# Kernel tuning notes

Hardware: AMD Instinct MI355X
Metric: run time of the kernel (lower is better)

Reference implementation:

```python
import jax, jax.numpy as jnp
import numpy as np

B, T, C, H = 1, 4096, 768, 12
D = C // H  # head_dim = 64


def setup_inputs() -> dict:
    key = jax.random.key(0)
    ks = jax.random.split(key, 5)
    s = 1.0 / np.sqrt(C)
    return {
        "x": jax.random.normal(ks[0], (B, T, C), dtype=jnp.float32),
        "Wq": jax.random.normal(ks[1], (C, C), dtype=jnp.float32) * s,
        "bq": jnp.zeros((C,), dtype=jnp.float32),
        "Wk": jax.random.normal(ks[2], (C, C), dtype=jnp.float32) * s,
        "bk": jnp.zeros((C,), dtype=jnp.float32),
        "Wv": jax.random.normal(ks[3], (C, C), dtype=jnp.float32) * s,
        "bv": jnp.zeros((C,), dtype=jnp.float32),
        "Wo": jax.random.normal(ks[4], (C, C), dtype=jnp.float32) * s,
        "bo": jnp.zeros((C,), dtype=jnp.float32),
    }


def reference(x, Wq, bq, Wk, bk, Wv, bv, Wo, bo):
    # Linear projections (torch nn.Linear: y = x @ W.T + b)
    q = (x @ Wq.T + bq).reshape(B, T, H, D).transpose(0, 2, 1, 3)  # [B,H,T,D]
    k = (x @ Wk.T + bk).reshape(B, T, H, D).transpose(0, 2, 1, 3)
    v = (x @ Wv.T + bv).reshape(B, T, H, D).transpose(0, 2, 1, 3)
    scale = 1.0 / jnp.sqrt(jnp.asarray(D, dtype=x.dtype))
    scores = jnp.einsum("bhqd,bhkd->bhqk", q, k) * scale  # [B,H,T,T]
    attn = jax.nn.softmax(scores, axis=-1)
    out = jnp.einsum("bhqk,bhkd->bhqd", attn, v)  # [B,H,T,D]
    y = out.transpose(0, 2, 1, 3).reshape(B, T, C)
    return y @ Wo.T + bo
```

## Files before the change

### kernel.cpp

```cpp
#include <hip/hip_runtime.h>
#include <math.h>

#define T_ 4096
#define C_ 768
#define H_ 12
#define D_ 64
#define TC_ ((size_t)T_ * C_)
#define CC_ ((size_t)C_ * C_)

typedef __attribute__((ext_vector_type(8))) __bf16 bf16x8;
typedef __attribute__((ext_vector_type(4))) __bf16 bf16x4;
typedef __attribute__((ext_vector_type(2))) __bf16 bf16x2;
typedef __attribute__((ext_vector_type(4))) float f32x4;
typedef __attribute__((ext_vector_type(16))) float f32x16;
typedef __attribute__((ext_vector_type(8))) unsigned short u16x8;
typedef __attribute__((ext_vector_type(4))) unsigned int u32x4;


static __device__ __forceinline__ float fast_exp2(float x) {
#if __has_builtin(__builtin_amdgcn_exp2f)
    return __builtin_amdgcn_exp2f(x);
#else
    return exp2f(x);
#endif
}

static __device__ __forceinline__ unsigned pack2(float a, float b) {
    bf16x2 v = { (__bf16)a, (__bf16)b };
    return __builtin_bit_cast(unsigned, v);
}

static __device__ __forceinline__ void gload16(const void* g, void* l) {
    __builtin_amdgcn_global_load_lds(
        (const __attribute__((address_space(1))) unsigned int*)g,
        (__attribute__((address_space(3))) unsigned int*)l, 16, 0, 0);
}

__global__ void f2b_kernel(const float* __restrict__ in,
                           unsigned short* __restrict__ out, int n4) {
    int i = blockIdx.x * blockDim.x + threadIdx.x;
    const int stride = gridDim.x * blockDim.x;
    for (; i < n4; i += stride) {
        float4 v = ((const float4*)in)[i];
        bf16x4 o = { (__bf16)v.x, (__bf16)v.y, (__bf16)v.z, (__bf16)v.w };
        *(bf16x4*)&out[(size_t)i * 4] = o;
    }
}

__global__ void f2b4_kernel(const float* __restrict__ w0, const float* __restrict__ w1,
                            const float* __restrict__ w2, const float* __restrict__ w3,
                            unsigned short* __restrict__ out) {
    const float* src = (blockIdx.y == 0) ? w0 : (blockIdx.y == 1) ? w1
                     : (blockIdx.y == 2) ? w2 : w3;
    unsigned short* dst = out + (size_t)blockIdx.y * CC_;
    const int i = blockIdx.x * blockDim.x + threadIdx.x;
    float4 v = ((const float4*)src)[i];
    bf16x4 o = { (__bf16)v.x, (__bf16)v.y, (__bf16)v.z, (__bf16)v.w };
    *(bf16x4*)&dst[(size_t)i * 4] = o;
}

#define BM 128
#define BN 128
#define BKG 64

struct GemmRegs {
    const unsigned short* ag[4];
    const unsigned short* wg[4];
    unsigned short* la[4];
    unsigned short* lw[4];
    int lq, lg, wr, wc;
};

static __device__ __forceinline__ void gemm_setup(
    GemmRegs& R, const unsigned short* A, const unsigned short* W,
    unsigned short* Asm, unsigned short* Bsm, int bm, int bn, int K)
{
    const int tid = threadIdx.x;
    const int wave = tid >> 6, lane = tid & 63;
    R.lq = lane & 15; R.lg = lane >> 4;
    R.wr = wave >> 1; R.wc = wave & 1;
#pragma unroll
    for (int i = 0; i < 4; ++i) {
        const int flat = wave * 256 + i * 64 + lane;
        const int row = flat >> 3;
        const int col = ((flat & 7) * 8) ^ ((row & 7) << 3);
        R.ag[i] = A + (size_t)(bm + row) * K + col;
        R.wg[i] = W + (size_t)(bn + row) * K + col;
        R.la[i] = Asm + (wave * 4 + i) * 512;
        R.lw[i] = Bsm + (wave * 4 + i) * 512;
    }
}

static __device__ __forceinline__ void gemm_loop(
    GemmRegs& R, unsigned short* Asm, unsigned short* Bsm, int K, f32x4 acc[4][4])
{
    const int sw = (R.lq & 7) << 3;
    int colA[2];
#pragma unroll
    for (int ks = 0; ks < 2; ++ks)
        colA[ks] = (ks * 32 + R.lg * 8) ^ sw;
    for (int kb = 0; kb < K; kb += BKG) {
        __syncthreads();
#pragma unroll
        for (int i = 0; i < 4; ++i) {
            gload16(R.ag[i] + kb, R.la[i]);
            gload16(R.wg[i] + kb, R.lw[i]);
        }
        __syncthreads();
        __builtin_amdgcn_s_setprio(1);
#pragma unroll
        for (int ks = 0; ks < 2; ++ks) {
            bf16x8 af[4], wf[4];
#pragma unroll
            for (int m = 0; m < 4; ++m)
                af[m] = *(const bf16x8*)&Asm[(R.wr * 64 + m * 16 + R.lq) * BKG + colA[ks]];
#pragma unroll
            for (int n = 0; n < 4; ++n)
                wf[n] = *(const bf16x8*)&Bsm[(R.wc * 64 + n * 16 + R.lq) * BKG + colA[ks]];
#pragma unroll
            for (int m = 0; m < 4; ++m)
#pragma unroll
                for (int n = 0; n < 4; ++n)
                    acc[m][n] = __builtin_amdgcn_mfma_f32_16x16x32_bf16(af[m], wf[n], acc[m][n], 0, 0, 0);
        }
        __builtin_amdgcn_s_setprio(0);
    }
}

__global__ __launch_bounds__(256) void qkv128(
    const unsigned short* __restrict__ xb,
    const unsigned short* __restrict__ Wqb, const unsigned short* __restrict__ Wkb,
    const unsigned short* __restrict__ Wvb,
    const float* __restrict__ bq, const float* __restrict__ bk, const float* __restrict__ bv,
    unsigned short* __restrict__ Qb, unsigned short* __restrict__ Kb,
    unsigned short* __restrict__ Vtb)
{
    __shared__ unsigned short Asm[BM * BKG];
    __shared__ unsigned short Bsm[BN * BKG];
    const int z = blockIdx.z;
    const unsigned short* W = (z == 0) ? Wqb : (z == 1) ? Wkb : Wvb;
    const float* bias = (z == 0) ? bq : (z == 1) ? bk : bv;
    const int bm = blockIdx.x * BM, bn = blockIdx.y * BN;

    GemmRegs R;
    gemm_setup(R, xb, W, Asm, Bsm, bm, bn, C_);
    f32x4 acc[4][4] = {};
    gemm_loop(R, Asm, Bsm, C_, acc);

    const float sc = (z == 0) ? 0.18033688011112042f : 1.0f;
#pragma unroll
    for (int mt = 0; mt < 4; ++mt) {
        const int m0 = bm + R.wr * 64 + mt * 16 + R.lg * 4;
#pragma unroll
        for (int nt = 0; nt < 4; ++nt) {
            const int n = bn + R.wc * 64 + nt * 16 + R.lq;
            const float b = bias[n];
            if (z == 2) {
                const int tp = (m0 & ~12) | ((m0 & 4) << 1) | ((m0 & 8) >> 1);
                bf16x4 o = { (__bf16)(acc[mt][nt][0] + b), (__bf16)(acc[mt][nt][1] + b),
                             (__bf16)(acc[mt][nt][2] + b), (__bf16)(acc[mt][nt][3] + b) };
                *(bf16x4*)&Vtb[(size_t)n * T_ + tp] = o;
            } else {
                unsigned short* Y = (z == 0) ? Qb : Kb;
#pragma unroll
                for (int r = 0; r < 4; ++r)
                    Y[(size_t)(m0 + r) * C_ + n] =
                        __builtin_bit_cast(unsigned short, (__bf16)((acc[mt][nt][r] + b) * sc));
            }
        }
    }
}

__global__ __launch_bounds__(256) void out128(
    const unsigned short* __restrict__ ctxb, const unsigned short* __restrict__ Wob,
    const float* __restrict__ bo, float* __restrict__ out)
{
    __shared__ unsigned short Asm[BM * BKG];
    __shared__ unsigned short Bsm[BN * BKG];
    const int bm = blockIdx.x * BM, bn = blockIdx.y * BN;

    GemmRegs R;
    gemm_setup(R, ctxb, Wob, Asm, Bsm, bm, bn, C_);
    f32x4 acc[4][4] = {};
    gemm_loop(R, Asm, Bsm, C_, acc);

#pragma unroll
    for (int mt = 0; mt < 4; ++mt) {
        const int m0 = bm + R.wr * 64 + mt * 16 + R.lg * 4;
#pragma unroll
        for (int nt = 0; nt < 4; ++nt) {
            const int n = bn + R.wc * 64 + nt * 16 + R.lq;
            const float b = bo[n];
#pragma unroll
            for (int r = 0; r < 4; ++r)
                out[(size_t)(m0 + r) * C_ + n] = acc[mt][nt][r] + b;
        }
    }
}

#define SPLITS 2
#define KVTILES (T_ / 64 / SPLITS)

__global__ __launch_bounds__(256, 3) void attn32s(
    const unsigned short* __restrict__ Qb, const unsigned short* __restrict__ Kb,
    const unsigned short* __restrict__ Vtb, unsigned short* __restrict__ Opart,
    float* __restrict__ lpart)
{
    __shared__ unsigned short Ks[2][64 * 64];
    __shared__ unsigned short Vs[2][64 * 64];

    const int tid = threadIdx.x;
    const int wave = tid >> 6, lane = tid & 63;
    const int lq = lane & 31, hi = lane >> 5;

    const int bid = blockIdx.x;
    const int sw = (bid & 7) * 96 + (bid >> 3);
    const int split = sw / 384;
    const int rem = sw - split * 384;
    const int h = rem >> 5, qt = rem & 31;
    const int q0 = qt * 128 + wave * 32;
    const int kv0 = split * (T_ / SPLITS);

    const int swz = (lq & 7) << 4;
    int rof[4];
#pragma unroll
    for (int ks = 0; ks < 4; ++ks)
        rof[ks] = lq * 128 + ((hi * 16 + ks * 32) ^ swz);

    bf16x8 qf[4];
    {
        const unsigned short* qp = Qb + (size_t)(q0 + lq) * C_ + h * D_ + hi * 8;
#pragma unroll
        for (int ks = 0; ks < 4; ++ks) qf[ks] = *(const bf16x8*)(qp + ks * 16);
    }

    const char* gk[2];
    const char* gv[2];
    char* kds[2];
    char* vds[2];
#pragma unroll
    for (int j = 0; j < 2; ++j) {
        const int f = j * 256 + tid;
        const int row = f >> 3;
        const int col = (f & 7) * 16;
        gk[j] = (const char*)Kb + (size_t)(kv0 + row) * (C_ * 2) + h * (D_ * 2) + col;
        gv[j] = (const char*)Vtb + (size_t)(h * D_ + row) * (T_ * 2) + kv0 * 2 + col;
        kds[j] = (char*)&Ks[0][0] + row * 128 + (col ^ ((row & 7) << 4));
        vds[j] = (char*)&Vs[0][0] + row * 128 + (col ^ ((row & 7) << 4));
    }

    u16x8 kreg[2], vreg[2];
#pragma unroll
    for (int j = 0; j < 2; ++j) {
        kreg[j] = *(const u16x8*)(gk[j]);
        vreg[j] = *(const u16x8*)(gv[j]);
    }
#pragma unroll
    for (int j = 0; j < 2; ++j) {
        *(u16x8*)kds[j] = kreg[j];
        *(u16x8*)vds[j] = vreg[j];
    }
    __syncthreads();
#pragma unroll
    for (int j = 0; j < 2; ++j) {
        kreg[j] = *(const u16x8*)(gk[j] + 64 * (C_ * 2));
        vreg[j] = *(const u16x8*)(gv[j] + 128);
    }

    f32x16 oacc0 = {}, oacc1 = {};
    float lrun = 0.f;

    for (int it = 0; it < KVTILES; ++it) {
        const int cur = it & 1;
        const char* kb = (const char*)&Ks[cur][0];
        const char* vb = (const char*)&Vs[cur][0];

        f32x16 s0 = {}, s1 = {};
        __builtin_amdgcn_s_setprio(1);
#pragma unroll
        for (int ks = 0; ks < 4; ++ks) {
            bf16x8 kf0 = *(const bf16x8*)(kb + rof[ks]);
            bf16x8 kf1 = *(const bf16x8*)(kb + 4096 + rof[ks]);
            s0 = __builtin_amdgcn_mfma_f32_32x32x16_bf16(kf0, qf[ks], s0, 0, 0, 0);
            s1 = __builtin_amdgcn_mfma_f32_32x32x16_bf16(kf1, qf[ks], s1, 0, 0, 0);
        }
        __builtin_amdgcn_s_setprio(0);

#pragma unroll
        for (int r = 0; r < 16; ++r) {
            s0[r] = fast_exp2(s0[r]);
            s1[r] = fast_exp2(s1[r]);
        }
        {
            float ps[8];
#pragma unroll
            for (int r = 0; r < 8; ++r)
                ps[r] = (s0[r] + s0[r + 8]) + (s1[r] + s1[r + 8]);
            ps[0] += ps[4]; ps[1] += ps[5]; ps[2] += ps[6]; ps[3] += ps[7];
            float pt = (ps[0] + ps[1]) + (ps[2] + ps[3]);
            lrun += pt + __shfl_xor(pt, 32);
        }

        bf16x8 pf[4];
        {
            u32x4 a0 = { pack2(s0[0], s0[1]), pack2(s0[2], s0[3]),
                         pack2(s0[4], s0[5]), pack2(s0[6], s0[7]) };
            pf[0] = __builtin_bit_cast(bf16x8, a0);
            u32x4 a1 = { pack2(s0[8], s0[9]), pack2(s0[10], s0[11]),
                         pack2(s0[12], s0[13]), pack2(s0[14], s0[15]) };
            pf[1] = __builtin_bit_cast(bf16x8, a1);
            u32x4 a2 = { pack2(s1[0], s1[1]), pack2(s1[2], s1[3]),
                         pack2(s1[4], s1[5]), pack2(s1[6], s1[7]) };
            pf[2] = __builtin_bit_cast(bf16x8, a2);
            u32x4 a3 = { pack2(s1[8], s1[9]), pack2(s1[10], s1[11]),
                         pack2(s1[12], s1[13]), pack2(s1[14], s1[15]) };
            pf[3] = __builtin_bit_cast(bf16x8, a3);
        }

        __builtin_amdgcn_s_setprio(1);
#pragma unroll
        for (int ks = 0; ks < 4; ++ks) {
            bf16x8 vf0 = *(const bf16x8*)(vb + rof[ks]);
            bf16x8 vf1 = *(const bf16x8*)(vb + 4096 + rof[ks]);
            oacc0 = __builtin_amdgcn_mfma_f32_32x32x16_bf16(vf0, pf[ks], oacc0, 0, 0, 0);
            oacc1 = __builtin_amdgcn_mfma_f32_32x32x16_bf16(vf1, pf[ks], oacc1, 0, 0, 0);
        }
        __builtin_amdgcn_s_setprio(0);

        if (it + 1 < KVTILES) {
            const int nxt = (cur ^ 1) * 8192;
#pragma unroll
            for (int j = 0; j < 2; ++j) {
                *(u16x8*)(kds[j] + nxt) = kreg[j];
                *(u16x8*)(vds[j] + nxt) = vreg[j];
            }
            if (it + 2 < KVTILES) {
                const size_t ko = (size_t)(it + 2) * 64 * (C_ * 2);
                const size_t vo = (size_t)(it + 2) * 128;
#pragma unroll
                for (int j = 0; j < 2; ++j) {
                    kreg[j] = *(const u16x8*)(gk[j] + ko);
                    vreg[j] = *(const u16x8*)(gv[j] + vo);
                }
            }
        }
        __syncthreads();
    }

    unsigned short* op = Opart + ((size_t)(split * H_ + h) * T_ + q0 + lq) * 64;
#pragma unroll
    for (int k = 0; k < 4; ++k) {
        bf16x4 o0 = { (__bf16)oacc0[4 * k + 0], (__bf16)oacc0[4 * k + 1],
                      (__bf16)oacc0[4 * k + 2], (__bf16)oacc0[4 * k + 3] };
        *(bf16x4*)&op[8 * k + 4 * hi] = o0;
        bf16x4 o1 = { (__bf16)oacc1[4 * k + 0], (__bf16)oacc1[4 * k + 1],
                      (__bf16)oacc1[4 * k + 2], (__bf16)oacc1[4 * k + 3] };
        *(bf16x4*)&op[32 + 8 * k + 4 * hi] = o1;
    }
    if (hi == 0)
        lpart[(size_t)(split * H_ + h) * T_ + q0 + lq] = lrun;
}

__global__ __launch_bounds__(256) void combine2(
    const unsigned short* __restrict__ Opart, const float* __restrict__ lpart,
    unsigned short* __restrict__ ctxb)
{
    const int idx = blockIdx.x * 256 + threadIdx.x;
    const int dq = idx & 15;
    const int ht = idx >> 4;
    const int h = ht >> 12;
    const int t = ht & (T_ - 1);

    const float l0 = lpart[(size_t)h * T_ + t];
    const float l1 = lpart[(size_t)(H_ + h) * T_ + t];
    const float inv = 1.f / (l0 + l1);
    const bf16x4 a0 = *(const bf16x4*)&Opart[((size_t)h * T_ + t) * 64 + dq * 4];
    const bf16x4 a1 = *(const bf16x4*)&Opart[((size_t)(H_ + h) * T_ + t) * 64 + dq * 4];
    bf16x4 r;
#pragma unroll
    for (int i = 0; i < 4; ++i)
        r[i] = (__bf16)(((float)a0[i] + (float)a1[i]) * inv);
    *(bf16x4*)&ctxb[(size_t)t * C_ + h * D_ + dq * 4] = r;
}

extern "C" void kernel_launch(void* const* d_in, const int* in_sizes, int n_in,
                              void* d_out, int out_size, void* d_ws, size_t ws_size,
                              hipStream_t stream) {
    (void)in_sizes; (void)n_in; (void)out_size; (void)ws_size;
    const float* x  = (const float*)d_in[0];
    const float* Wq = (const float*)d_in[1];
    const float* bq = (const float*)d_in[2];
    const float* Wk = (const float*)d_in[3];
    const float* bk = (const float*)d_in[4];
    const float* Wv = (const float*)d_in[5];
    const float* bv = (const float*)d_in[6];
    const float* Wo = (const float*)d_in[7];
    const float* bo = (const float*)d_in[8];
    float* out = (float*)d_out;

    unsigned short* ws    = (unsigned short*)d_ws;
    unsigned short* xb    = ws;
    unsigned short* Wqb   = xb + TC_;
    unsigned short* Wkb   = Wqb + CC_;
    unsigned short* Wvb   = Wkb + CC_;
    unsigned short* Wob   = Wvb + CC_;
    unsigned short* Qb    = Wob + CC_;
    unsigned short* Kb    = Qb + TC_;
    unsigned short* Vtb   = Kb + TC_;
    unsigned short* ctxb  = Vtb + TC_;
    unsigned short* Opart = ctxb + TC_;
    float* lpart = (float*)(Opart + 2 * TC_);

    f2b_kernel<<<2048, 256, 0, stream>>>(x, xb, (int)(TC_ / 4));
    dim3 gw(CC_ / 4 / 256, 4);
    f2b4_kernel<<<gw, 256, 0, stream>>>(Wq, Wk, Wv, Wo, Wqb);

    dim3 gq(T_ / BM, C_ / BN, 3);
    qkv128<<<gq, 256, 0, stream>>>(xb, Wqb, Wkb, Wvb, bq, bk, bv, Qb, Kb, Vtb);

    attn32s<<<768, 256, 0, stream>>>(Qb, Kb, Vtb, Opart, lpart);
    combine2<<<(T_ * H_ * 16) / 256, 256, 0, stream>>>(Opart, lpart, ctxb);

    dim3 go(T_ / BM, C_ / BN);
    out128<<<go, 256, 0, stream>>>(ctxb, Wob, bo, out);
}
```

Baseline: 119.7 us.

## Fuse split-KV combine into output projection GEMM and allow four KV splits

```diff
diff --git a/kernel.cpp b/kernel.cpp
--- a/kernel.cpp
+++ b/kernel.cpp
@@ -22,6 +22,14 @@
     return __builtin_amdgcn_exp2f(x);
 #else
     return exp2f(x);
+#endif
+}
+
+static __device__ __forceinline__ float fast_rcp(float x) {
+#if __has_builtin(__builtin_amdgcn_rcpf)
+    return __builtin_amdgcn_rcpf(x);
+#else
+    return 1.0f / x;
 #endif
 }
 
@@ -91,6 +99,29 @@
     }
 }
 
+static __device__ __forceinline__ void gemm_mfma_step(
+    GemmRegs& R, unsigned short* Asm, unsigned short* Bsm,
+    const int colA[2], f32x4 acc[4][4])
+{
+    __builtin_amdgcn_s_setprio(1);
+#pragma unroll
+    for (int ks = 0; ks < 2; ++ks) {
+        bf16x8 af[4], wf[4];
+#pragma unroll
+        for (int m = 0; m < 4; ++m)
+            af[m] = *(const bf16x8*)&Asm[(R.wr * 64 + m * 16 + R.lq) * BKG + colA[ks]];
+#pragma unroll
+        for (int n = 0; n < 4; ++n)
+            wf[n] = *(const bf16x8*)&Bsm[(R.wc * 64 + n * 16 + R.lq) * BKG + colA[ks]];
+#pragma unroll
+        for (int m = 0; m < 4; ++m)
+#pragma unroll
+            for (int n = 0; n < 4; ++n)
+                acc[m][n] = __builtin_amdgcn_mfma_f32_16x16x32_bf16(af[m], wf[n], acc[m][n], 0, 0, 0);
+    }
+    __builtin_amdgcn_s_setprio(0);
+}
+
 static __device__ __forceinline__ void gemm_loop(
     GemmRegs& R, unsigned short* Asm, unsigned short* Bsm, int K, f32x4 acc[4][4])
 {
@@ -107,23 +138,7 @@
             gload16(R.wg[i] + kb, R.lw[i]);
         }
         __syncthreads();
-        __builtin_amdgcn_s_setprio(1);
-#pragma unroll
-        for (int ks = 0; ks < 2; ++ks) {
-            bf16x8 af[4], wf[4];
-#pragma unroll
-            for (int m = 0; m < 4; ++m)
-                af[m] = *(const bf16x8*)&Asm[(R.wr * 64 + m * 16 + R.lq) * BKG + colA[ks]];
-#pragma unroll
-            for (int n = 0; n < 4; ++n)
-                wf[n] = *(const bf16x8*)&Bsm[(R.wc * 64 + n * 16 + R.lq) * BKG + colA[ks]];
-#pragma unroll
-            for (int m = 0; m < 4; ++m)
-#pragma unroll
-                for (int n = 0; n < 4; ++n)
-                    acc[m][n] = __builtin_amdgcn_mfma_f32_16x16x32_bf16(af[m], wf[n], acc[m][n], 0, 0, 0);
-        }
-        __builtin_amdgcn_s_setprio(0);
+        gemm_mfma_step(R, Asm, Bsm, colA, acc);
     }
 }
 
@@ -171,25 +186,104 @@
     }
 }
 
-__global__ __launch_bounds__(256) void out128(
-    const unsigned short* __restrict__ ctxb, const unsigned short* __restrict__ Wob,
-    const float* __restrict__ bo, float* __restrict__ out)
+template <int S>
+__global__ __launch_bounds__(256) void outc128(
+    const unsigned short* __restrict__ Opart, const float* __restrict__ lpart,
+    const unsigned short* __restrict__ Wob, const float* __restrict__ bo,
+    float* __restrict__ out)
 {
     __shared__ unsigned short Asm[BM * BKG];
     __shared__ unsigned short Bsm[BN * BKG];
+    const int tid = threadIdx.x;
+    const int wave = tid >> 6, lane = tid & 63;
+    const int lq = lane & 15, lg = lane >> 4;
+    const int wr = wave >> 1, wc = wave & 1;
     const int bm = blockIdx.x * BM, bn = blockIdx.y * BN;
 
-    GemmRegs R;
-    gemm_setup(R, ctxb, Wob, Asm, Bsm, bm, bn, C_);
+    int trow[4], d0[4];
+    unsigned short* lda[4];
+    const unsigned short* wg[4];
+    unsigned short* lw[4];
+#pragma unroll
+    for (int i = 0; i < 4; ++i) {
+        const int flat = wave * 256 + i * 64 + lane;
+        const int row = flat >> 3;
+        trow[i] = bm + row;
+        d0[i] = (((flat & 7) ^ (row & 7)) * 8);
+        lda[i] = Asm + (size_t)flat * 8;
+        const int colw = ((flat & 7) * 8) ^ ((row & 7) << 3);
+        wg[i] = Wob + (size_t)(bn + row) * C_ + colw;
+        lw[i] = Bsm + (wave * 4 + i) * 512;
+    }
+    const int sw = (lq & 7) << 3;
+    int colA[2];
+#pragma unroll
+    for (int ks = 0; ks < 2; ++ks)
+        colA[ks] = (ks * 32 + lg * 8) ^ sw;
+
     f32x4 acc[4][4] = {};
-    gemm_loop(R, Asm, Bsm, C_, acc);
+
+    u16x8 oreg[4][S];
+    float lv[4];
+#pragma unroll
+    for (int i = 0; i < 4; ++i) {
+        float lsum = 0.f;
+#pragma unroll
+        for (int s = 0; s < S; ++s) {
+            oreg[i][s] = *(const u16x8*)(Opart + ((size_t)(s * H_) * T_ + trow[i]) * 64 + d0[i]);
+            lsum += lpart[(size_t)(s * H_) * T_ + trow[i]];
+        }
+        lv[i] = lsum;
+    }
+
+    for (int kb = 0; kb < C_; kb += BKG) {
+        __syncthreads();
+#pragma unroll
+        for (int i = 0; i < 4; ++i) {
+            const float inv = fast_rcp(lv[i]);
+            const bf16x8 b0 = __builtin_bit_cast(bf16x8, oreg[i][0]);
+            float v[8];
+#pragma unroll
+            for (int j = 0; j < 8; ++j) v[j] = (float)b0[j];
+#pragma unroll
+            for (int s = 1; s < S; ++s) {
+                const bf16x8 bs = __builtin_bit_cast(bf16x8, oreg[i][s]);
+#pragma unroll
+                for (int j = 0; j < 8; ++j) v[j] += (float)bs[j];
+            }
+            u32x4 pk = { pack2(v[0] * inv, v[1] * inv), pack2(v[2] * inv, v[3] * inv),
+                         pack2(v[4] * inv, v[5] * inv), pack2(v[6] * inv, v[7] * inv) };
+            *(u32x4*)lda[i] = pk;
+            gload16(wg[i] + kb, lw[i]);
+        }
+        __syncthreads();
+
+        if (kb + BKG < C_) {
+            const int hn = (kb >> 6) + 1;
+#pragma unroll
+            for (int i = 0; i < 4; ++i) {
+                float lsum = 0.f;
+#pragma unroll
+                for (int s = 0; s < S; ++s) {
+                    oreg[i][s] = *(const u16x8*)(Opart +
+                        ((size_t)(s * H_ + hn) * T_ + trow[i]) * 64 + d0[i]);
+                    lsum += lpart[(size_t)(s * H_ + hn) * T_ + trow[i]];
+                }
+                lv[i] = lsum;
+            }
+        }
+
+        GemmRegs R;
+        R.lq = lq; R.lg = lg; R.wr = wr; R.wc = wc;
+        gemm_mfma_step(R, Asm, Bsm, colA, acc);
+    }
 
 #pragma unroll
     for (int mt = 0; mt < 4; ++mt) {
-        const int m0 = bm + R.wr * 64 + mt * 16 + R.lg * 4;
+        const int m0 = bm + wr * 64 + mt * 16 + lg * 4;
 #pragma unroll
         for (int nt = 0; nt < 4; ++nt) {
-            const int n = bn + R.wc * 64 + nt * 16 + R.lq;
+            const int n = bn + wc * 64 + nt * 16 + lq;
             const float b = bo[n];
 #pragma unroll
             for (int r = 0; r < 4; ++r)
@@ -198,9 +292,7 @@
     }
 }
 
-#define SPLITS 2
-#define KVTILES (T_ / 64 / SPLITS)
-
+template <int S>
 __global__ __launch_bounds__(256, 3) void attn32s(
     const unsigned short* __restrict__ Qb, const unsigned short* __restrict__ Kb,
     const unsigned short* __restrict__ Vtb, unsigned short* __restrict__ Opart,
@@ -213,13 +305,15 @@
     const int wave = tid >> 6, lane = tid & 63;
     const int lq = lane & 31, hi = lane >> 5;
 
+    const int perx = (S * 384) / 8;
     const int bid = blockIdx.x;
-    const int sw = (bid & 7) * 96 + (bid >> 3);
+    const int sw = (bid & 7) * perx + (bid >> 3);
     const int split = sw / 384;
     const int rem = sw - split * 384;
     const int h = rem >> 5, qt = rem & 31;
     const int q0 = qt * 128 + wave * 32;
-    const int kv0 = split * (T_ / SPLITS);
+    const int kv0 = split * (T_ / S);
+    const int KVTILES = T_ / 64 / S;
 
     const int swz = (lq & 7) << 4;
     int rof[4];
@@ -361,32 +455,10 @@
         lpart[(size_t)(split * H_ + h) * T_ + q0 + lq] = lrun;
 }
 
-__global__ __launch_bounds__(256) void combine2(
-    const unsigned short* __restrict__ Opart, const float* __restrict__ lpart,
-    unsigned short* __restrict__ ctxb)
-{
-    const int idx = blockIdx.x * 256 + threadIdx.x;
-    const int dq = idx & 15;
-    const int ht = idx >> 4;
-    const int h = ht >> 12;
-    const int t = ht & (T_ - 1);
-
-    const float l0 = lpart[(size_t)h * T_ + t];
-    const float l1 = lpart[(size_t)(H_ + h) * T_ + t];
-    const float inv = 1.f / (l0 + l1);
-    const bf16x4 a0 = *(const bf16x4*)&Opart[((size_t)h * T_ + t) * 64 + dq * 4];
-    const bf16x4 a1 = *(const bf16x4*)&Opart[((size_t)(H_ + h) * T_ + t) * 64 + dq * 4];
-    bf16x4 r;
-#pragma unroll
-    for (int i = 0; i < 4; ++i)
-        r[i] = (__bf16)(((float)a0[i] + (float)a1[i]) * inv);
-    *(bf16x4*)&ctxb[(size_t)t * C_ + h * D_ + dq * 4] = r;
-}
-
 extern "C" void kernel_launch(void* const* d_in, const int* in_sizes, int n_in,
                               void* d_out, int out_size, void* d_ws, size_t ws_size,
                               hipStream_t stream) {
-    (void)in_sizes; (void)n_in; (void)out_size; (void)ws_size;
+    (void)in_sizes; (void)n_in; (void)out_size;
     const float* x  = (const float*)d_in[0];
     const float* Wq = (const float*)d_in[1];
     const float* bq = (const float*)d_in[2];
@@ -407,9 +479,11 @@
     unsigned short* Qb    = Wob + CC_;
     unsigned short* Kb    = Qb + TC_;
     unsigned short* Vtb   = Kb + TC_;
-    unsigned short* ctxb  = Vtb + TC_;
-    unsigned short* Opart = ctxb + TC_;
-    float* lpart = (float*)(Opart + 2 * TC_);
+    unsigned short* Opart = Vtb + TC_;
+
+    const size_t lsz = (size_t)H_ * T_ * sizeof(float);
+    const size_t need4 = (size_t)(8 * TC_ + 4 * CC_) * 2 + 4 * lsz;
+    const int S = (ws_size >= need4) ? 4 : 2;
 
     f2b_kernel<<<2048, 256, 0, stream>>>(x, xb, (int)(TC_ / 4));
     dim3 gw(CC_ / 4 / 256, 4);
@@ -418,9 +492,14 @@
     dim3 gq(T_ / BM, C_ / BN, 3);
     qkv128<<<gq, 256, 0, stream>>>(xb, Wqb, Wkb, Wvb, bq, bk, bv, Qb, Kb, Vtb);
 
-    attn32s<<<768, 256, 0, stream>>>(Qb, Kb, Vtb, Opart, lpart);
-    combine2<<<(T_ * H_ * 16) / 256, 256, 0, stream>>>(Opart, lpart, ctxb);
-
     dim3 go(T_ / BM, C_ / BN);
-    out128<<<go, 256, 0, stream>>>(ctxb, Wob, bo, out);
-}
+    if (S == 4) {
+        float* lpart = (float*)(Opart + 4 * TC_);
+        attn32s<4><<<4 * 384, 256, 0, stream>>>(Qb, Kb, Vtb, Opart, lpart);
+        outc128<4><<<go, 256, 0, stream>>>(Opart, lpart, Wob, bo, out);
+    } else {
+        float* lpart = (float*)(Opart + 2 * TC_);
+        attn32s<2><<<2 * 384, 256, 0, stream>>>(Qb, Kb, Vtb, Opart, lpart);
+        outc128<2><<<go, 256, 0, stream>>>(Opart, lpart, Wob, bo, out);
+    }
+}
```

After: 129.8 us. +8.5%, slower.
